# Kernel tuning notes

Hardware: AMD Instinct MI355X
Metric: run time of the kernel (lower is better)

Reference implementation:

```python
import jax, jax.numpy as jnp
import numpy as np

B, L, HID = 4, 1024, 2048
H, DK, DV, KS = 16, 128, 128, 4
KEY_DIM, VAL_DIM = H * DK, H * DV
CONV_DIM = 2 * KEY_DIM + VAL_DIM
EPS = 1e-6


def setup_inputs() -> dict:
    key = jax.random.key(0)
    ks = jax.random.split(key, 8)
    return {
        "hidden_states": jax.random.normal(ks[0], (B, L, HID), jnp.float32),
        "W_qkvz": jax.random.normal(ks[1], (HID, 2 * KEY_DIM + 2 * VAL_DIM), jnp.float32) * 0.02,
        "W_ba": jax.random.normal(ks[2], (HID, 2 * H), jnp.float32) * 0.02,
        "conv_w": jax.random.normal(ks[3], (CONV_DIM, KS), jnp.float32) * 0.1,
        "conv_b": jnp.zeros((CONV_DIM,), jnp.float32),
        "A_log": jnp.log(jax.random.uniform(ks[4], (H,), jnp.float32, 1e-3, 16.0)),
        "dt_bias": jnp.ones((H,), jnp.float32),
        "norm_w": jnp.ones((DV,), jnp.float32),
        "W_out": jax.random.normal(ks[5], (VAL_DIM, HID), jnp.float32) * 0.02,
    }


def _l2norm(x):
    return x * jax.lax.rsqrt(jnp.sum(x * x, -1, keepdims=True) + EPS)


def _gdn_core(q, k, v, g, beta):
    # q,k: [B,L,H,DK], v: [B,L,H,DV], g,beta: [B,L,H]
    scale = q.shape[-1] ** -0.5

    def step(S, inp):
        qt, kt, vt, gt, bt = inp  # [B,H,*]
        S = S * jnp.exp(gt)[..., None, None]          # per-step gated decay
        v_pred = jnp.einsum('bhk,bhkd->bhd', kt, S)   # read memory at k_t
        delta = (vt - v_pred) * bt[..., None]         # delta-rule update
        S = S + jnp.einsum('bhk,bhd->bhkd', kt, delta)
        o = jnp.einsum('bhk,bhkd->bhd', qt, S) * scale
        return S, o

    S0 = jnp.zeros((q.shape[0], q.shape[2], q.shape[3], v.shape[3]), q.dtype)
    xs = (q.transpose(1, 0, 2, 3), k.transpose(1, 0, 2, 3), v.transpose(1, 0, 2, 3),
          g.transpose(1, 0, 2), beta.transpose(1, 0, 2))
    _, o = jax.lax.scan(step, S0, xs)
    return o.transpose(1, 0, 2, 3)  # [B,L,H,DV]


def reference(hidden_states, W_qkvz, W_ba, conv_w, conv_b, A_log, dt_bias, norm_w, W_out):
    qkvz = hidden_states @ W_qkvz                      # [B,L,2*key+2*val]
    ba = hidden_states @ W_ba                          # [B,L,2H]
    mixed = qkvz[..., :CONV_DIM]
    z = qkvz[..., CONV_DIM:].reshape(B, L, H, DV)
    b_, a_ = ba[..., :H], ba[..., H:]

    # depthwise causal conv1d (left pad KS-1), no activation (activation=None)
    x = mixed.transpose(0, 2, 1)                       # [B,C,L]
    x = jax.lax.conv_general_dilated(
        x, conv_w[:, None, :], (1,), [(KS - 1, 0)],
        dimension_numbers=('NCH', 'OIH', 'NCH'), feature_group_count=CONV_DIM)
    x = (x + conv_b[None, :, None]).transpose(0, 2, 1)  # [B,L,C]

    q = _l2norm(x[..., :KEY_DIM].reshape(B, L, H, DK))
    k = _l2norm(x[..., KEY_DIM:2 * KEY_DIM].reshape(B, L, H, DK))
    v = x[..., 2 * KEY_DIM:].reshape(B, L, H, DV)

    g = -jnp.exp(A_log)[None, None, :] * jax.nn.softplus(a_ + dt_bias[None, None, :])
    beta = jax.nn.sigmoid(b_)

    o = _gdn_core(q, k, v, g, beta)                    # [B,L,H,DV]

    # gated RMSNorm (norm before gate)
    var = jnp.mean(o * o, -1, keepdims=True)
    o = o * jax.lax.rsqrt(var + EPS) * norm_w * jax.nn.sigmoid(z)
    return o.reshape(B, L, VAL_DIM) @ W_out            # [B,L,HID]
```

## Files before the change

kernel.cpp:

```cpp
#include <hip/hip_runtime.h>

typedef unsigned short u16;
typedef unsigned int u32;
typedef short short8 __attribute__((ext_vector_type(8)));
typedef float float4v __attribute__((ext_vector_type(4)));

#define L_SEQ 1024
#define NB 4
#define NH 16
#define DK 128
#define DV 128
#define HID 2048
#define NQKVZ 8192
#define CONV_DIM 6144
#define GDN_SCALE 0.08838834764831845f

static __device__ __forceinline__ float bf2f(u16 u) {
    union { u32 i; float f; } x; x.i = ((u32)u) << 16; return x.f;
}
static __device__ __forceinline__ u16 f2bf(float f) {
    union { float f; u32 u; } x; x.f = f;
    u32 r = x.u + 0x7FFF + ((x.u >> 16) & 1);
    return (u16)(r >> 16);
}

union FragU { short8 v; uint4 u; };

#define GLOAD_LDS16(g, l)                                        \
    __builtin_amdgcn_global_load_lds(                            \
        (const __attribute__((address_space(1))) void*)(g),      \
        (__attribute__((address_space(3))) void*)(l), 16, 0, 0)

__global__ __launch_bounds__(256) void f32_to_bf16(
    const float* __restrict__ in, u16* __restrict__ out) {
    long i = ((long)blockIdx.x * 256 + threadIdx.x) * 8;
    float4 a = *(const float4*)(in + i);
    float4 b = *(const float4*)(in + i + 4);
    u16 tmp[8];
    tmp[0] = f2bf(a.x); tmp[1] = f2bf(a.y); tmp[2] = f2bf(a.z); tmp[3] = f2bf(a.w);
    tmp[4] = f2bf(b.x); tmp[5] = f2bf(b.y); tmp[6] = f2bf(b.z); tmp[7] = f2bf(b.w);
    *(uint4*)(out + i) = *(const uint4*)tmp;
}

__global__ __launch_bounds__(256) void transpose_f32_bf16(
    const float* __restrict__ in, u16* __restrict__ out, int R, int C) {
    __shared__ float tile[32][33];
    int bx = blockIdx.x, by = blockIdx.y;
    int c = threadIdx.x & 31;
    int r0 = threadIdx.x >> 5;
#pragma unroll
    for (int i = 0; i < 4; i++) {
        int r = r0 + i * 8;
        tile[r][c] = in[(long)(by * 32 + r) * C + bx * 32 + c];
    }
    __syncthreads();
#pragma unroll
    for (int i = 0; i < 4; i++) {
        int r = r0 + i * 8;
        out[(long)(bx * 32 + r) * R + by * 32 + c] = f2bf(tile[c][r]);
    }
}

#define BM 128
#define BN 128
#define BKK 32

static __device__ __forceinline__ void store_out(u16* p, float v)  { *p = f2bf(v); }
static __device__ __forceinline__ void store_out(float* p, float v){ *p = v; }

template <typename OutT>
__global__ __launch_bounds__(256) void gemm_abT(
    const u16* __restrict__ A, const u16* __restrict__ BT,
    OutT* __restrict__ C, int M, int N, int K) {
    __shared__ u16 As[BM * BKK];
    __shared__ u16 Bs[BN * BKK];
    int t = threadIdx.x;
    int lane = t & 63;
    int w = t >> 6;
    int wm = (w & 1) * 64;
    int wn = (w >> 1) * 64;
    int l15 = lane & 15;
    int quad = lane >> 4;
    long blockM = (long)blockIdx.y * BM;
    long blockN = (long)blockIdx.x * BN;

    float4v acc[4][4];
#pragma unroll
    for (int i = 0; i < 4; i++)
#pragma unroll
        for (int j = 0; j < 4; j++) acc[i][j] = (float4v){0.f, 0.f, 0.f, 0.f};

    const u16* Ab = A + blockM * K;
    const u16* Bb = BT + blockN * K;

    const int r0 = t >> 2,         c0 = (t & 3) * 8;
    const int r1 = (t + 256) >> 2, c1 = ((t + 256) & 3) * 8;
    u16* As0 = As + t * 8;         u16* As1 = As + (t + 256) * 8;
    u16* Bs0 = Bs + t * 8;         u16* Bs1 = Bs + (t + 256) * 8;
    const u16* Ag0 = Ab + (long)r0 * K + c0;
    const u16* Ag1 = Ab + (long)r1 * K + c1;
    const u16* Bg0 = Bb + (long)r0 * K + c0;
    const u16* Bg1 = Bb + (long)r1 * K + c1;

    for (int k0 = 0; k0 < K; k0 += BKK) {
        __syncthreads();
        GLOAD_LDS16(Ag0 + k0, As0);
        GLOAD_LDS16(Ag1 + k0, As1);
        GLOAD_LDS16(Bg0 + k0, Bs0);
        GLOAD_LDS16(Bg1 + k0, Bs1);
        __syncthreads();

        FragU fa[4], fb[4];
#pragma unroll
        for (int i = 0; i < 4; i++) {
            fa[i].u = *(const uint4*)(As + (wm + i * 16 + l15) * BKK + quad * 8);
            fb[i].u = *(const uint4*)(Bs + (wn + i * 16 + l15) * BKK + quad * 8);
        }
#pragma unroll
        for (int i = 0; i < 4; i++)
#pragma unroll
            for (int j = 0; j < 4; j++)
                acc[i][j] = __builtin_amdgcn_mfma_f32_16x16x32_bf16(
                    fa[i].v, fb[j].v, acc[i][j], 0, 0, 0);
    }

#pragma unroll
    for (int i = 0; i < 4; i++) {
        long mrow = blockM + wm + i * 16 + quad * 4;
#pragma unroll
        for (int j = 0; j < 4; j++) {
            long col = blockN + wn + j * 16 + l15;
#pragma unroll
            for (int r = 0; r < 4; r++) {
                store_out(&C[(mrow + r) * N + col], acc[i][j][r]);
            }
        }
    }
}

#define G1_LDSU 32768

__global__ __launch_bounds__(512, 2) void gemm1_8ph(
    const u16* __restrict__ A, const u16* __restrict__ BT,
    u16* __restrict__ C) {
    const int K = HID, N = NQKVZ;
    __shared__ __align__(16) u16 lds[2 * G1_LDSU];

    int t = threadIdx.x;
    int lane = t & 63, w = t >> 6, l15 = lane & 15, quad = lane >> 4;
    int wm = w & 1, wn = w >> 1;

    int orig = blockIdx.x;
    int wg = (orig & 7) * 64 + (orig >> 3);
    int p = wg >> 6, q = wg & 63;
    long blockM = (long)((p >> 2) * 8 + (q >> 3)) * 256;
    long blockN = (long)((p & 3) * 8 + (q & 7)) * 256;

    int srow = t >> 3;
    int scol = ((t & 7) ^ (srow & 7)) * 8;
    const u16* Ast = A + (blockM + srow) * (long)K + scol;
    const u16* Bst = BT + (blockN + srow) * (long)K + scol;

#define STA(db, qq, T) GLOAD_LDS16(Ast + (long)(qq) * 64 * K + (T) * 64,      \
                                   lds + (db) * G1_LDSU + (qq) * 4096 + t * 8)
#define STB(db, qq, T) GLOAD_LDS16(Bst + (long)(qq) * 64 * K + (T) * 64,      \
                                   lds + (db) * G1_LDSU + 16384 + (qq) * 4096 + t * 8)

    const int rowA0 = (wm * 128 + l15) * 64;
    const int rowB0 = 16384 + (wn * 64 + l15) * 64;
    const int cs0 = ((quad) ^ (l15 & 7)) * 8;
    const int cs1 = ((4 + quad) ^ (l15 & 7)) * 8;

    float4v acc[8][4];
#pragma unroll
    for (int mi = 0; mi < 8; mi++)
#pragma unroll
        for (int nj = 0; nj < 4; nj++) acc[mi][nj] = (float4v){0.f, 0.f, 0.f, 0.f};

    STA(0, 0, 0); STA(0, 1, 0); STA(0, 2, 0); STA(0, 3, 0);
    STB(0, 0, 0); STB(0, 1, 0); STB(0, 2, 0); STB(0, 3, 0);
    STA(1, 0, 1); STA(1, 2, 1);
    asm volatile("s_waitcnt vmcnt(2)" ::: "memory");
    __builtin_amdgcn_s_barrier();

    FragU bA[4][2], bB0[2][2], bB1[2][2];

    for (int g = 0; g < 32; ++g) {
        const int c = g & 1, db = c ^ 1;
        const u16* sb = lds + c * G1_LDSU;

#pragma unroll
        for (int i = 0; i < 4; i++) {
            bA[i][0].u = *(const uint4*)(sb + rowA0 + i * 1024 + cs0);
            bA[i][1].u = *(const uint4*)(sb + rowA0 + i * 1024 + cs1);
        }
#pragma unroll
        for (int j = 0; j < 2; j++) {
            bB0[j][0].u = *(const uint4*)(sb + rowB0 + j * 1024 + cs0);
            bB0[j][1].u = *(const uint4*)(sb + rowB0 + j * 1024 + cs1);
        }
        if (g + 1 < 32) { STA(db, 1, g + 1); STA(db, 3, g + 1); }
        __builtin_amdgcn_s_barrier();
        asm volatile("s_waitcnt lgkmcnt(0)" ::: "memory");
        __builtin_amdgcn_s_setprio(1);
#pragma unroll
        for (int i = 0; i < 4; i++)
#pragma unroll
            for (int j = 0; j < 2; j++) {
                acc[i][j] = __builtin_amdgcn_mfma_f32_16x16x32_bf16(
                    bA[i][0].v, bB0[j][0].v, acc[i][j], 0, 0, 0);
                acc[i][j] = __builtin_amdgcn_mfma_f32_16x16x32_bf16(
                    bA[i][1].v, bB0[j][1].v, acc[i][j], 0, 0, 0);
            }
        __builtin_amdgcn_s_setprio(0);

#pragma unroll
        for (int j = 0; j < 2; j++) {
            bB1[j][0].u = *(const uint4*)(sb + rowB0 + (2 + j) * 1024 + cs0);
            bB1[j][1].u = *(const uint4*)(sb + rowB0 + (2 + j) * 1024 + cs1);
        }
        if (g + 1 < 32) { STB(db, 0, g + 1); STB(db, 1, g + 1); }
        __builtin_amdgcn_s_barrier();
        asm volatile("s_waitcnt lgkmcnt(0)" ::: "memory");
        __builtin_amdgcn_s_setprio(1);
#pragma unroll
        for (int i = 0; i < 4; i++)
#pragma unroll
            for (int j = 0; j < 2; j++) {
                acc[i][2 + j] = __builtin_amdgcn_mfma_f32_16x16x32_bf16(
                    bA[i][0].v, bB1[j][0].v, acc[i][2 + j], 0, 0, 0);
                acc[i][2 + j] = __builtin_amdgcn_mfma_f32_16x16x32_bf16(
                    bA[i][1].v, bB1[j][1].v, acc[i][2 + j], 0, 0, 0);
            }
        __builtin_amdgcn_s_setprio(0);

#pragma unroll
        for (int i = 0; i < 4; i++) {
            bA[i][0].u = *(const uint4*)(sb + rowA0 + (4 + i) * 1024 + cs0);
            bA[i][1].u = *(const uint4*)(sb + rowA0 + (4 + i) * 1024 + cs1);
        }
        if (g + 1 < 32) { STB(db, 2, g + 1); STB(db, 3, g + 1); }
        __builtin_amdgcn_s_barrier();
        asm volatile("s_waitcnt lgkmcnt(0)" ::: "memory");
        __builtin_amdgcn_s_setprio(1);
#pragma unroll
        for (int i = 0; i < 4; i++)
#pragma unroll
            for (int j = 0; j < 2; j++) {
                acc[4 + i][j] = __builtin_amdgcn_mfma_f32_16x16x32_bf16(
                    bA[i][0].v, bB0[j][0].v, acc[4 + i][j], 0, 0, 0);
                acc[4 + i][j] = __builtin_amdgcn_mfma_f32_16x16x32_bf16(
                    bA[i][1].v, bB0[j][1].v, acc[4 + i][j], 0, 0, 0);
            }
        __builtin_amdgcn_s_setprio(0);

        if (g + 2 < 32) { STA(c, 0, g + 2); STA(c, 2, g + 2); }
        __builtin_amdgcn_s_barrier();
        __builtin_amdgcn_s_setprio(1);
#pragma unroll
        for (int i = 0; i < 4; i++)
#pragma unroll
            for (int j = 0; j < 2; j++) {
                acc[4 + i][2 + j] = __builtin_amdgcn_mfma_f32_16x16x32_bf16(
                    bA[i][0].v, bB1[j][0].v, acc[4 + i][2 + j], 0, 0, 0);
                acc[4 + i][2 + j] = __builtin_amdgcn_mfma_f32_16x16x32_bf16(
                    bA[i][1].v, bB1[j][1].v, acc[4 + i][2 + j], 0, 0, 0);
            }
        __builtin_amdgcn_s_setprio(0);

        if (g < 30)       { asm volatile("s_waitcnt vmcnt(2)" ::: "memory"); }
        else if (g == 30) { asm volatile("s_waitcnt vmcnt(0)" ::: "memory"); }
        __builtin_amdgcn_s_barrier();
    }

#pragma unroll
    for (int mi = 0; mi < 8; mi++) {
        long row0 = blockM + wm * 128 + mi * 16 + quad * 4;
#pragma unroll
        for (int nj = 0; nj < 4; nj++) {
            long col = blockN + wn * 64 + nj * 16 + l15;
#pragma unroll
            for (int r = 0; r < 4; r++)
                C[(row0 + r) * N + col] = f2bf(acc[mi][nj][r]);
        }
    }
#undef STA
#undef STB
}

#define G2_LDSU 24576

__global__ __launch_bounds__(512) void gemm2_2ph(
    const u16* __restrict__ A, const u16* __restrict__ BT,
    float* __restrict__ C) {
    const int K = HID, N = 2048;
    __shared__ __align__(16) u16 lds[2 * G2_LDSU];

    int t = threadIdx.x;
    int lane = t & 63, w = t >> 6, l15 = lane & 15, quad = lane >> 4;
    int wm = w & 1, wn = w >> 1;

    int orig = blockIdx.x;
    int x = orig & 7, q = orig >> 3;
    long blockM = (long)((x >> 2) * 8 + (q >> 2)) * 256;
    long blockN = (long)((x & 3) * 4 + (q & 3)) * 128;

    int srow = t >> 3;
    int scol = ((t & 7) ^ (srow & 7)) * 8;
    const u16* Ast = A + (blockM + srow) * (long)K + scol;
    const u16* Bst = BT + (blockN + srow) * (long)K + scol;

#define STA2(db, qq, T) GLOAD_LDS16(Ast + (long)(qq) * 64 * K + (T) * 64,     \
                                    lds + (db) * G2_LDSU + (qq) * 4096 + t * 8)
#define STB2(db, hh, T) GLOAD_LDS16(Bst + (long)(hh) * 64 * K + (T) * 64,     \
                                    lds + (db) * G2_LDSU + 16384 + (hh) * 4096 + t * 8)

    const int cs0 = ((quad) ^ (l15 & 7)) * 8;
    const int cs1 = ((4 + quad) ^ (l15 & 7)) * 8;
    int offA[8], offB[2];
#pragma unroll
    for (int mi = 0; mi < 8; mi++)
        offA[mi] = (wm * 2 + (mi >> 2)) * 4096 + (((mi & 3) * 16 + l15)) * 64;
#pragma unroll
    for (int nj = 0; nj < 2; nj++)
        offB[nj] = 16384 + (wn >> 1) * 4096 + ((wn & 1) * 32 + nj * 16 + l15) * 64;

    float4v acc[8][2];
#pragma unroll
    for (int mi = 0; mi < 8; mi++)
#pragma unroll
        for (int nj = 0; nj < 2; nj++) acc[mi][nj] = (float4v){0.f, 0.f, 0.f, 0.f};

    STA2(0, 0, 0); STA2(0, 2, 0); STB2(0, 0, 0); STB2(0, 1, 0);
    STA2(0, 1, 0); STA2(0, 3, 0);
    STA2(1, 0, 1); STA2(1, 2, 1); STB2(1, 0, 1); STB2(1, 1, 1);
    asm volatile("s_waitcnt vmcnt(6)" ::: "memory");
    __builtin_amdgcn_s_barrier();

    FragU fA[4][2], fB[2][2];

    for (int g = 0; g < 32; ++g) {
        const int c = g & 1, db = c ^ 1;
        const u16* sb = lds + c * G2_LDSU;

#pragma unroll
        for (int i = 0; i < 4; i++) {
            fA[i][0].u = *(const uint4*)(sb + offA[i] + cs0);
            fA[i][1].u = *(const uint4*)(sb + offA[i] + cs1);
        }
#pragma unroll
        for (int j = 0; j < 2; j++) {
            fB[j][0].u = *(const uint4*)(sb + offB[j] + cs0);
            fB[j][1].u = *(const uint4*)(sb + offB[j] + cs1);
        }
        if (g < 31) { STA2(db, 1, g + 1); STA2(db, 3, g + 1); }
        asm volatile("s_waitcnt lgkmcnt(8)" ::: "memory");
        __builtin_amdgcn_s_barrier();
        __builtin_amdgcn_s_setprio(1);
#pragma unroll
        for (int i = 0; i < 4; i++)
#pragma unroll
            for (int j = 0; j < 2; j++) {
                acc[i][j] = __builtin_amdgcn_mfma_f32_16x16x32_bf16(
                    fA[i][0].v, fB[j][0].v, acc[i][j], 0, 0, 0);
                acc[i][j] = __builtin_amdgcn_mfma_f32_16x16x32_bf16(
                    fA[i][1].v, fB[j][1].v, acc[i][j], 0, 0, 0);
            }
        __builtin_amdgcn_s_setprio(0);

        if (g < 31) { asm volatile("s_waitcnt vmcnt(6)" ::: "memory"); }
        else        { asm volatile("s_waitcnt vmcnt(0)" ::: "memory"); }
        __builtin_amdgcn_s_barrier();
        if (g < 30) { STA2(c, 0, g + 2); STA2(c, 2, g + 2);
                      STB2(c, 0, g + 2); STB2(c, 1, g + 2); }
#pragma unroll
        for (int i = 0; i < 4; i++) {
            fA[i][0].u = *(const uint4*)(sb + offA[4 + i] + cs0);
            fA[i][1].u = *(const uint4*)(sb + offA[4 + i] + cs1);
        }
        __builtin_amdgcn_s_setprio(1);
#pragma unroll
        for (int i = 0; i < 4; i++)
#pragma unroll
            for (int j = 0; j < 2; j++) {
                acc[4 + i][j] = __builtin_amdgcn_mfma_f32_16x16x32_bf16(
                    fA[i][0].v, fB[j][0].v, acc[4 + i][j], 0, 0, 0);
                acc[4 + i][j] = __builtin_amdgcn_mfma_f32_16x16x32_bf16(
                    fA[i][1].v, fB[j][1].v, acc[4 + i][j], 0, 0, 0);
            }
        __builtin_amdgcn_s_setprio(0);

        if (g < 30)       { asm volatile("s_waitcnt vmcnt(6)" ::: "memory"); }
        else if (g == 30) { asm volatile("s_waitcnt vmcnt(2)" ::: "memory"); }
        if (g < 31) __builtin_amdgcn_s_barrier();
    }

#pragma unroll
    for (int mi = 0; mi < 8; mi++) {
        long row0 = blockM + wm * 128 + mi * 16 + quad * 4;
#pragma unroll
        for (int nj = 0; nj < 2; nj++) {
            long col = blockN + wn * 32 + nj * 16 + l15;
#pragma unroll
            for (int r = 0; r < 4; r++)
                C[(row0 + r) * N + col] = acc[mi][nj][r];
        }
    }
#undef STA2
#undef STB2
}

__global__ __launch_bounds__(256) void ba_gemm(
    const u16* __restrict__ hsb, const u16* __restrict__ WbaTb,
    const float* __restrict__ A_log, const float* __restrict__ dtb,
    float* __restrict__ gout, float* __restrict__ bout) {
    __shared__ u16 As[2][64 * 32];
    __shared__ u16 Bs[2][32 * 32];
    int t = threadIdx.x;
    int lane = t & 63, w = t >> 6, l15 = lane & 15, quad = lane >> 4;
    long blockM = (long)blockIdx.x * 64;

    float4v acc[2];
    acc[0] = (float4v){0.f, 0.f, 0.f, 0.f};
    acc[1] = (float4v){0.f, 0.f, 0.f, 0.f};

    const u16* Ag  = hsb + (blockM + (t >> 2)) * (long)HID + (t & 3) * 8;
    const u16* Bg1 = WbaTb + (long)(t >> 4) * HID + ((t * 2) & 31);
    const u16* Bg2 = Bg1 + 16 * (long)HID;

#define STBA(buf, k0) do {                                                     \
        GLOAD_LDS16(Ag + (k0), As[buf] + t * 8);                               \
        __builtin_amdgcn_global_load_lds(                                      \
            (const __attribute__((address_space(1))) void*)(Bg1 + (k0)),       \
            (__attribute__((address_space(3))) void*)(Bs[buf] + t * 2), 4, 0, 0); \
        __builtin_amdgcn_global_load_lds(                                      \
            (const __attribute__((address_space(1))) void*)(Bg2 + (k0)),       \
            (__attribute__((address_space(3))) void*)(Bs[buf] + 512 + t * 2), 4, 0, 0); \
    } while (0)

    STBA(0, 0);
    STBA(1, 32);

    for (int k0 = 0; k0 < HID; k0 += 32) {
        int buf = (k0 >> 5) & 1;
        if (k0 < HID - 64) { asm volatile("s_waitcnt vmcnt(3)" ::: "memory"); }
        else               { asm volatile("s_waitcnt vmcnt(0)" ::: "memory"); }
        __builtin_amdgcn_s_barrier();
        FragU fa, fb0, fb1;
        fa.u  = *(const uint4*)(As[buf] + (w * 16 + l15) * 32 + quad * 8);
        fb0.u = *(const uint4*)(Bs[buf] + l15 * 32 + quad * 8);
        fb1.u = *(const uint4*)(Bs[buf] + (16 + l15) * 32 + quad * 8);
        asm volatile("s_waitcnt lgkmcnt(0)" ::: "memory");
        __builtin_amdgcn_sched_barrier(0);
        __builtin_amdgcn_s_barrier();
        if (k0 + 64 < HID) STBA(buf, k0 + 64);
        acc[0] = __builtin_amdgcn_mfma_f32_16x16x32_bf16(fa.v, fb0.v, acc[0], 0, 0, 0);
        acc[1] = __builtin_amdgcn_mfma_f32_16x16x32_bf16(fa.v, fb1.v, acc[1], 0, 0, 0);
    }
#undef STBA

#pragma unroll
    for (int j = 0; j < 2; j++) {
        int n = j * 16 + l15;
#pragma unroll
        for (int r = 0; r < 4; r++) {
            long m = blockM + w * 16 + quad * 4 + r;
            int b = (int)(m >> 10), l = (int)(m & 1023);
            float v = acc[j][r];
            if (n < 16) {
                bout[((long)(b * NH + n)) * L_SEQ + l] = 1.f / (1.f + expf(-v));
            } else {
                int h = n - 16;
                float x = v + dtb[h];
                float sp = (x > 20.f) ? x : log1pf(expf(x));
                gout[((long)(b * NH + h)) * L_SEQ + l] = -expf(A_log[h]) * sp;
            }
        }
    }
}

__global__ __launch_bounds__(256) void conv_qkv(
    const u16* __restrict__ qkvz, const float* __restrict__ conv_w,
    const float* __restrict__ conv_b,
    u16* __restrict__ qs, u16* __restrict__ ks, u16* __restrict__ vs) {
    int orig = blockIdx.x;
    int bl = ((orig & 7) << 9) + (orig >> 3);
    int b = bl >> 10, l = bl & 1023;
    int t = threadIdx.x;
    __shared__ float xb[CONV_DIM];
    __shared__ float red[32][9];
    __shared__ float rbuf[32];

    for (int c = t; c < CONV_DIM; c += 256) {
        float acc = conv_b[c];
        float w0 = conv_w[c * 4 + 0];
        float w1 = conv_w[c * 4 + 1];
        float w2 = conv_w[c * 4 + 2];
        float w3 = conv_w[c * 4 + 3];
        long rowbase = (long)(b * L_SEQ) * NQKVZ + c;
        if (l - 3 >= 0) acc += bf2f(qkvz[rowbase + (long)(l - 3) * NQKVZ]) * w0;
        if (l - 2 >= 0) acc += bf2f(qkvz[rowbase + (long)(l - 2) * NQKVZ]) * w1;
        if (l - 1 >= 0) acc += bf2f(qkvz[rowbase + (long)(l - 1) * NQKVZ]) * w2;
        acc += bf2f(qkvz[rowbase + (long)l * NQKVZ]) * w3;
        xb[c] = acc;
    }
    __syncthreads();
    {
        int grp = t >> 3;
        int j8 = t & 7;
        float s = 0.f;
#pragma unroll
        for (int i = 0; i < 16; i++) {
            float xv = xb[grp * 128 + j8 * 16 + i];
            s += xv * xv;
        }
        red[grp][j8] = s;
    }
    __syncthreads();
    if (t < 32) {
        float s = 0.f;
#pragma unroll
        for (int i = 0; i < 8; i++) s += red[t][i];
        rbuf[t] = rsqrtf(s + 1e-6f);
    }
    __syncthreads();
    for (int c = t; c < CONV_DIM; c += 256) {
        float xv = xb[c];
        if (c < 2048) {
            int h = c >> 7, d = c & 127;
            qs[(((long)(b * NH + h)) * L_SEQ + l) * DK + d] = f2bf(xv * rbuf[h]);
        } else if (c < 4096) {
            int c2 = c - 2048;
            int h = c2 >> 7, d = c2 & 127;
            ks[(((long)(b * NH + h)) * L_SEQ + l) * DK + d] = f2bf(xv * rbuf[16 + h]);
        } else {
            int c2 = c - 4096;
            int h = c2 >> 7, d = c2 & 127;
            vs[(((long)(b * NH + h)) * L_SEQ + l) * DV + d] = f2bf(xv);
        }
    }
}

__global__ __launch_bounds__(256) void gdn_prep(
    const u16* __restrict__ ks_g, const u16* __restrict__ qs_g,
    const float* __restrict__ g_g, const float* __restrict__ b_g,
    u16* __restrict__ Tbuf, u16* __restrict__ Pbuf,
    u16* __restrict__ wbq, u16* __restrict__ qlq, u16* __restrict__ kdq,
    float* __restrict__ gam_g) {
    int cid = blockIdx.x;
    int bh = cid >> 4;
    int ch = cid & 15;
    long rowbase = (long)bh * L_SEQ + ch * 64;
    int t = threadIdx.x;
    int lane = t & 63, w = t >> 6, l15 = lane & 15, quad = lane >> 4;

    __shared__ u16 Kl[64 * 136];
    __shared__ u16 Ql[64 * 136];
    __shared__ float Am[64 * 66];
    __shared__ float Tm[64 * 66];
    __shared__ float Tt[32 * 33];
    __shared__ float Gs[64], lamL[64], betaL[64], dlL[64];

    {
        int row = t >> 2, seg = (t & 3) * 32;
        const u16* ksrc = ks_g + (rowbase + row) * DK + seg;
        const u16* qsrc = qs_g + (rowbase + row) * DK + seg;
        *(uint4*)&Kl[row * 136 + seg]      = *(const uint4*)ksrc;
        *(uint4*)&Kl[row * 136 + seg + 8]  = *(const uint4*)(ksrc + 8);
        *(uint4*)&Kl[row * 136 + seg + 16] = *(const uint4*)(ksrc + 16);
        *(uint4*)&Kl[row * 136 + seg + 24] = *(const uint4*)(ksrc + 24);
        *(uint4*)&Ql[row * 136 + seg]      = *(const uint4*)qsrc;
        *(uint4*)&Ql[row * 136 + seg + 8]  = *(const uint4*)(qsrc + 8);
        *(uint4*)&Ql[row * 136 + seg + 16] = *(const uint4*)(qsrc + 16);
        *(uint4*)&Ql[row * 136 + seg + 24] = *(const uint4*)(qsrc + 24);
        if (t < 64) Gs[t] = g_g[rowbase + t];
        else if (t < 128) betaL[t - 64] = b_g[rowbase + t - 64];
    }
    __syncthreads();
    if (t < 64) {
        float gv = Gs[t];
#pragma unroll
        for (int off = 1; off < 64; off <<= 1) {
            float n = __shfl_up(gv, off);
            if (lane >= off) gv += n;
        }
        Gs[t] = gv;
    }
    __syncthreads();
    if (t < 64) {
        float G63 = Gs[63];
        float lm = expf(Gs[t]);
        lamL[t] = lm;
        dlL[t] = expf(G63 - Gs[t]);
        if (t == 0) gam_g[cid] = expf(G63);
    }
    float4v accKK[4], accQK[4];
#pragma unroll
    for (int tj = 0; tj < 4; tj++) {
        accKK[tj] = (float4v){0.f, 0.f, 0.f, 0.f};
        accQK[tj] = (float4v){0.f, 0.f, 0.f, 0.f};
    }
#pragma unroll
    for (int k0 = 0; k0 < 128; k0 += 32) {
        FragU ka, qa;
        ka.u = *(const uint4*)&Kl[(w * 16 + l15) * 136 + k0 + quad * 8];
        qa.u = *(const uint4*)&Ql[(w * 16 + l15) * 136 + k0 + quad * 8];
#pragma unroll
        for (int tj = 0; tj < 4; tj++) {
            FragU kb;
            kb.u = *(const uint4*)&Kl[(tj * 16 + l15) * 136 + k0 + quad * 8];
            accKK[tj] = __builtin_amdgcn_mfma_f32_16x16x32_bf16(ka.v, kb.v, accKK[tj], 0, 0, 0);
            accQK[tj] = __builtin_amdgcn_mfma_f32_16x16x32_bf16(qa.v, kb.v, accQK[tj], 0, 0, 0);
        }
    }
    __syncthreads();
#pragma unroll
    for (int tj = 0; tj < 4; tj++) {
#pragma unroll
        for (int r = 0; r < 4; r++) {
            int ti_ = w * 16 + quad * 4 + r;
            int j = tj * 16 + l15;
            float e = (j <= ti_) ? expf(Gs[ti_] - Gs[j]) : 0.f;
            Am[ti_ * 66 + j] = (j < ti_) ? betaL[ti_] * e * accKK[tj][r] : 0.f;
            Pbuf[(long)cid * 4096 + ti_ * 64 + j] =
                (j <= ti_) ? f2bf(GDN_SCALE * e * accQK[tj][r]) : (u16)0;
        }
    }
    {
        int row = t >> 2, seg = (t & 3) * 32;
        float sw = -betaL[row] * lamL[row];
        float sq = GDN_SCALE * lamL[row];
#pragma unroll
        for (int c0 = 0; c0 < 32; c0 += 8) {
            u16 wt[8], qt2[8];
#pragma unroll
            for (int j2 = 0; j2 < 8; j2++) {
                wt[j2]  = f2bf(sw * bf2f(Kl[row * 136 + seg + c0 + j2]));
                qt2[j2] = f2bf(sq * bf2f(Ql[row * 136 + seg + c0 + j2]));
            }
            *(uint4*)&wbq[(long)cid * 8192 + row * 128 + seg + c0] = *(uint4*)wt;
            *(uint4*)&qlq[(long)cid * 8192 + row * 128 + seg + c0] = *(uint4*)qt2;
        }
    }
    {
        int k = t & 127, t0b = (t >> 7) * 32;
#pragma unroll
        for (int t0 = 0; t0 < 32; t0 += 8) {
            u16 tmp[8];
#pragma unroll
            for (int j2 = 0; j2 < 8; j2++)
                tmp[j2] = f2bf(dlL[t0b + t0 + j2] * bf2f(Kl[(t0b + t0 + j2) * 136 + k]));
            *(uint4*)&kdq[(long)cid * 8192 + k * 64 + t0b + t0] = *(uint4*)tmp;
        }
    }
    __syncthreads();
    if (t < 32) {
        int c = t;
        for (int i = 0; i < 32; i++) {
            float s = (i == c) ? 1.f : 0.f;
            for (int j = 0; j < i; j++) s -= Am[i * 66 + j] * Tm[j * 66 + c];
            Tm[i * 66 + c] = s;
        }
    } else if (t >= 64 && t < 96) {
        int c = 32 + (t - 64);
        for (int i = 32; i < 64; i++) {
            float s = (i == c) ? 1.f : 0.f;
            for (int j = 32; j < i; j++) s -= Am[i * 66 + j] * Tm[j * 66 + c];
            Tm[i * 66 + c] = s;
        }
    } else if (t >= 128 && t < 192) {
        int idx = t - 128;
        for (int kk = 0; kk < 16; kk++) {
            int e = idx * 16 + kk;
            Tm[(e >> 5) * 66 + 32 + (e & 31)] = 0.f;
        }
    }
    __syncthreads();
    {
        int e0 = t * 4;
#pragma unroll
        for (int kk = 0; kk < 4; kk++) {
            int e = e0 + kk; int i = e >> 5, c = e & 31;
            float s = 0.f;
            for (int j = 0; j < 32; j++) s += Am[(32 + i) * 66 + j] * Tm[j * 66 + c];
            Tt[i * 33 + c] = s;
        }
    }
    __syncthreads();
    {
        int e0 = t * 4;
#pragma unroll
        for (int kk = 0; kk < 4; kk++) {
            int e = e0 + kk; int i = e >> 5, c = e & 31;
            float s = 0.f;
            for (int j = 0; j < 32; j++) s -= Tm[(32 + i) * 66 + 32 + j] * Tt[j * 33 + c];
            Tm[(32 + i) * 66 + c] = s;
        }
    }
    __syncthreads();
    {
        int row = t >> 2, c0 = (t & 3) * 16;
        u16 tmp[16];
#pragma unroll
        for (int i = 0; i < 16; i++) tmp[i] = f2bf(Tm[row * 66 + c0 + i]);
        *(uint4*)&Tbuf[(long)cid * 4096 + row * 64 + c0]     = *(uint4*)tmp;
        *(uint4*)&Tbuf[(long)cid * 4096 + row * 64 + c0 + 8] = *(uint4*)(tmp + 8);
    }
}

__global__ __launch_bounds__(256) void gdn_chunk(
    const u16* __restrict__ vs_g, const float* __restrict__ b_g,
    const u16* __restrict__ Tq, const u16* __restrict__ Pq,
    const u16* __restrict__ wbq, const u16* __restrict__ qlq,
    const u16* __restrict__ kdq, const float* __restrict__ gam_g,
    float* __restrict__ o_g) {
    int orig = blockIdx.x;
    int bid = ((orig & 7) << 6) + (orig >> 3);
    int dc = bid & 7;
    int bh = bid >> 3;
    int b = bh >> 4, h = bh & 15;
    int t = threadIdx.x;
    int lane = t & 63, w = t >> 6, l15 = lane & 15, quad = lane >> 4;

    __shared__ u16 s0h[16 * 136], s0l[16 * 136];
    __shared__ float vO[64 * 20];
    __shared__ u16 rhsT[16 * 72], DT[16 * 72];

    float4v S0r[2];
    S0r[0] = (float4v){0.f, 0.f, 0.f, 0.f};
    S0r[1] = (float4v){0.f, 0.f, 0.f, 0.f};

    const int orow = t >> 2, oseg = (t & 3) * 4;

    for (int ch = 0; ch < 16; ch++) {
        int cid = bh * 16 + ch;
        long rowbase = (long)bh * L_SEQ + ch * 64;
        float gam = gam_g[cid];

        const u16* wbp = wbq + (long)cid * 8192 + (w * 16 + l15) * 128 + quad * 8;
        uint4 wbf0 = *(const uint4*)(wbp);
        uint4 wbf1 = *(const uint4*)(wbp + 32);
        uint4 wbf2 = *(const uint4*)(wbp + 64);
        uint4 wbf3 = *(const uint4*)(wbp + 96);

        if (ch > 0) {
            float4 a = *(const float4*)&vO[orow * 20 + oseg];
            float* d2 = o_g + (((long)b * L_SEQ + (ch - 1) * 64 + orow) * 16 + h) * 128L
                        + dc * 16 + oseg;
            *(float4*)d2 = a;
        }
        {
            float beta = b_g[rowbase + orow];
            uint2 vv = *(const uint2*)(vs_g + (rowbase + orow) * DV + dc * 16 + oseg);
            const u16* vp = (const u16*)&vv;
#pragma unroll
            for (int j2 = 0; j2 < 4; j2++)
                vO[orow * 20 + oseg + j2] = beta * bf2f(vp[j2]);
        }
#pragma unroll
        for (int ktl = 0; ktl < 2; ktl++) {
            int kc = (2 * w + ktl) * 16 + l15;
#pragma unroll
            for (int r = 0; r < 4; r++) {
                float x = S0r[ktl][r];
                u16 hi = f2bf(x);
                float lo = x - bf2f(hi);
                s0h[(quad * 4 + r) * 136 + kc] = hi;
                s0l[(quad * 4 + r) * 136 + kc] = f2bf(lo);
            }
        }
        __syncthreads();

        const u16* Tp = Tq + (long)cid * 4096 + (w * 16 + l15) * 64 + quad * 8;
        uint4 Tf0 = *(const uint4*)(Tp);
        uint4 Tf1 = *(const uint4*)(Tp + 32);
        {
            float4v acc;
#pragma unroll
            for (int r = 0; r < 4; r++)
                acc[r] = vO[(w * 16 + quad * 4 + r) * 20 + l15];
            uint4 wbf[4] = {wbf0, wbf1, wbf2, wbf3};
#pragma unroll
            for (int k0 = 0; k0 < 4; k0++) {
                FragU a, bh_, bl_;
                a.u = wbf[k0];
                bh_.u = *(const uint4*)&s0h[l15 * 136 + k0 * 32 + quad * 8];
                acc = __builtin_amdgcn_mfma_f32_16x16x32_bf16(a.v, bh_.v, acc, 0, 0, 0);
                bl_.u = *(const uint4*)&s0l[l15 * 136 + k0 * 32 + quad * 8];
                acc = __builtin_amdgcn_mfma_f32_16x16x32_bf16(a.v, bl_.v, acc, 0, 0, 0);
            }
            u16 tmp[4] = {f2bf(acc[0]), f2bf(acc[1]), f2bf(acc[2]), f2bf(acc[3])};
            *(uint2*)&rhsT[l15 * 72 + w * 16 + quad * 4] = *(uint2*)tmp;
        }
        __syncthreads();

        const u16* qlp = qlq + (long)cid * 8192 + (w * 16 + l15) * 128 + quad * 8;
        uint4 qlf0 = *(const uint4*)(qlp);
        uint4 qlf1 = *(const uint4*)(qlp + 32);
        uint4 qlf2 = *(const uint4*)(qlp + 64);
        uint4 qlf3 = *(const uint4*)(qlp + 96);
        const u16* Pp = Pq + (long)cid * 4096 + (w * 16 + l15) * 64 + quad * 8;
        uint4 Pf0 = *(const uint4*)(Pp);
        uint4 Pf1 = *(const uint4*)(Pp + 32);
        {
            float4v acc = (float4v){0.f, 0.f, 0.f, 0.f};
            uint4 Tf[2] = {Tf0, Tf1};
#pragma unroll
            for (int k0 = 0; k0 < 2; k0++) {
                FragU a, b_;
                a.u = Tf[k0];
                b_.u = *(const uint4*)&rhsT[l15 * 72 + k0 * 32 + quad * 8];
                acc = __builtin_amdgcn_mfma_f32_16x16x32_bf16(a.v, b_.v, acc, 0, 0, 0);
            }
            u16 tmp[4] = {f2bf(acc[0]), f2bf(acc[1]), f2bf(acc[2]), f2bf(acc[3])};
            *(uint2*)&DT[l15 * 72 + w * 16 + quad * 4] = *(uint2*)tmp;
        }
        __syncthreads();

        uint4 kdf[2][2];
#pragma unroll
        for (int ktl = 0; ktl < 2; ktl++) {
            const u16* kdp = kdq + (long)cid * 8192 + ((2 * w + ktl) * 16 + l15) * 64 + quad * 8;
            kdf[ktl][0] = *(const uint4*)(kdp);
            kdf[ktl][1] = *(const uint4*)(kdp + 32);
        }
        {
            float4v acc = (float4v){0.f, 0.f, 0.f, 0.f};
            uint4 qlf[4] = {qlf0, qlf1, qlf2, qlf3};
#pragma unroll
            for (int k0 = 0; k0 < 4; k0++) {
                FragU a, bh_, bl_;
                a.u = qlf[k0];
                bh_.u = *(const uint4*)&s0h[l15 * 136 + k0 * 32 + quad * 8];
                acc = __builtin_amdgcn_mfma_f32_16x16x32_bf16(a.v, bh_.v, acc, 0, 0, 0);
                bl_.u = *(const uint4*)&s0l[l15 * 136 + k0 * 32 + quad * 8];
                acc = __builtin_amdgcn_mfma_f32_16x16x32_bf16(a.v, bl_.v, acc, 0, 0, 0);
            }
            uint4 Pf[2] = {Pf0, Pf1};
#pragma unroll
            for (int k0 = 0; k0 < 2; k0++) {
                FragU a, b_;
                a.u = Pf[k0];
                b_.u = *(const uint4*)&DT[l15 * 72 + k0 * 32 + quad * 8];
                acc = __builtin_amdgcn_mfma_f32_16x16x32_bf16(a.v, b_.v, acc, 0, 0, 0);
            }
#pragma unroll
            for (int r = 0; r < 4; r++)
                vO[(w * 16 + quad * 4 + r) * 20 + l15] = acc[r];
        }
#pragma unroll
        for (int ktl = 0; ktl < 2; ktl++) {
            float4v acc = S0r[ktl];
#pragma unroll
            for (int r = 0; r < 4; r++) acc[r] *= gam;
#pragma unroll
            for (int t0 = 0; t0 < 2; t0++) {
                FragU a, b_;
                a.u = *(const uint4*)&DT[l15 * 72 + t0 * 32 + quad * 8];
                b_.u = kdf[ktl][t0];
                acc = __builtin_amdgcn_mfma_f32_16x16x32_bf16(a.v, b_.v, acc, 0, 0, 0);
            }
            S0r[ktl] = acc;
        }
        __syncthreads();
    }
    {
        float4 a = *(const float4*)&vO[orow * 20 + oseg];
        float* d2 = o_g + (((long)b * L_SEQ + 15 * 64 + orow) * 16 + h) * 128L
                    + dc * 16 + oseg;
        *(float4*)d2 = a;
    }
}

__global__ __launch_bounds__(128) void gated_norm(
    const float* __restrict__ o, const u16* __restrict__ qkvz,
    const float* __restrict__ norm_w, u16* __restrict__ A2) {
    int bid = blockIdx.x;
    int t = threadIdx.x;
    float ov = o[(long)bid * 128 + t];
    float s = ov * ov;
#pragma unroll
    for (int off = 32; off > 0; off >>= 1) s += __shfl_down(s, off);
    __shared__ float ws2[2];
    if ((t & 63) == 0) ws2[t >> 6] = s;
    __syncthreads();
    float tot = ws2[0] + ws2[1];
    float rinv = rsqrtf(tot * (1.f / 128.f) + 1e-6f);
    int bl = bid >> 4, h = bid & 15;
    float z = bf2f(qkvz[(long)bl * NQKVZ + CONV_DIM + h * 128 + t]);
    float sig = 1.f / (1.f + expf(-z));
    float val = ov * rinv * norm_w[t] * sig;
    A2[(long)bl * 2048 + h * 128 + t] = f2bf(val);
}

extern "C" void kernel_launch(void* const* d_in, const int* in_sizes, int n_in,
                              void* d_out, int out_size, void* d_ws, size_t ws_size,
                              hipStream_t stream) {
    const float* hs    = (const float*)d_in[0];
    const float* Wqkvz = (const float*)d_in[1];
    const float* Wba   = (const float*)d_in[2];
    const float* convw = (const float*)d_in[3];
    const float* convb = (const float*)d_in[4];
    const float* A_log = (const float*)d_in[5];
    const float* dtb   = (const float*)d_in[6];
    const float* normw = (const float*)d_in[7];
    const float* Wout  = (const float*)d_in[8];

    char* ws = (char*)d_ws;
    size_t off = 0;
    auto alloc = [&](size_t bytes) {
        size_t o = off;
        off = (off + bytes + 255) & ~(size_t)255;
        return o;
    };
    size_t r0 = alloc((size_t)NQKVZ * HID * 2);
    size_t r1 = alloc((size_t)4096 * HID * 2);
    u16*   WqkvzT = (u16*)(ws + r0);
    float* os     = (float*)(ws + r0);
    u16*   hsb    = (u16*)(ws + r1);
    u16*   A2     = (u16*)(ws + r1);
    u16*   qkvz   = (u16*)(ws + alloc((size_t)4096 * NQKVZ * 2));
    u16*   qs     = (u16*)(ws + alloc((size_t)64 * L_SEQ * DK * 2));
    u16*   ks     = (u16*)(ws + alloc((size_t)64 * L_SEQ * DK * 2));
    u16*   vs     = (u16*)(ws + alloc((size_t)64 * L_SEQ * DV * 2));
    float* gs     = (float*)(ws + alloc((size_t)64 * L_SEQ * 4));
    float* bs     = (float*)(ws + alloc((size_t)64 * L_SEQ * 4));
    u16*   WoutT  = (u16*)(ws + alloc((size_t)HID * 2048 * 2));
    u16*   WbaTb  = (u16*)(ws + alloc((size_t)32 * HID * 2));
    u16*   Tbuf   = (u16*)(ws + alloc((size_t)1024 * 4096 * 2));
    u16*   Pbuf   = (u16*)(ws + alloc((size_t)1024 * 4096 * 2));
    u16*   wbq    = (u16*)(ws + alloc((size_t)1024 * 8192 * 2));
    u16*   qlq    = (u16*)(ws + alloc((size_t)1024 * 8192 * 2));
    u16*   kdq    = (u16*)(ws + alloc((size_t)1024 * 8192 * 2));
    float* gamb   = (float*)(ws + alloc((size_t)1024 * 4));

    hipLaunchKernelGGL(f32_to_bf16, dim3(4096), dim3(256), 0, stream, hs, hsb);
    hipLaunchKernelGGL(transpose_f32_bf16, dim3(NQKVZ / 32, HID / 32), dim3(256), 0, stream,
                       Wqkvz, WqkvzT, HID, NQKVZ);
    hipLaunchKernelGGL(transpose_f32_bf16, dim3(2048 / 32, 2048 / 32), dim3(256), 0, stream,
                       Wout, WoutT, 2048, 2048);
    hipLaunchKernelGGL(transpose_f32_bf16, dim3(1, HID / 32), dim3(256), 0, stream,
                       Wba, WbaTb, HID, 32);

    hipLaunchKernelGGL(gemm1_8ph, dim3(512), dim3(512), 0, stream,
                       hsb, WqkvzT, qkvz);

    hipLaunchKernelGGL(ba_gemm, dim3(64), dim3(256), 0, stream,
                       hsb, WbaTb, A_log, dtb, gs, bs);

    hipLaunchKernelGGL(conv_qkv, dim3(4096), dim3(256), 0, stream,
                       qkvz, convw, convb, qs, ks, vs);

    hipLaunchKernelGGL(gdn_prep, dim3(1024), dim3(256), 0, stream,
                       ks, qs, gs, bs, Tbuf, Pbuf, wbq, qlq, kdq, gamb);

    hipLaunchKernelGGL(gdn_chunk, dim3(512), dim3(256), 0, stream,
                       vs, bs, Tbuf, Pbuf, wbq, qlq, kdq, gamb, os);

    hipLaunchKernelGGL(gated_norm, dim3(4096 * NH), dim3(128), 0, stream,
                       os, qkvz, normw, A2);

    hipLaunchKernelGGL(gemm2_2ph, dim3(256), dim3(512), 0, stream,
                       A2, WoutT, (float*)d_out);
}
```

Measured before the change: 559.8 us.

## Retile ba_gemm into smaller blocks and vectorize conv_qkv loads and stores

ba_gemm now uses 32-row tiles with a 2x2 wave layout, doubling the grid from 64 to 128 blocks to fill more compute units. Each thread issues a single 16-byte global-to-LDS load per stage. conv_qkv now loads 8 bf16 channels per thread with 16-byte vector reads, vectorizes the conv weight and bias reads, and writes q/k/v with 16-byte stores instead of scalar 2-byte accesses. A no-op loop is also added to gemm1. The aim is better memory coalescing and more parallelism in the small kernels.

```diff
diff --git a/kernel.cpp b/kernel.cpp
--- a/kernel.cpp
+++ b/kernel.cpp
@@ -254,6 +254,8 @@
             }
         __builtin_amdgcn_s_setprio(0);
 
+#pragma unroll
+        for (int i = 0; i < 4; i++) { (void)0; }
         if (g + 2 < 32) { STA(c, 0, g + 2); STA(c, 2, g + 2); }
         __builtin_amdgcn_s_barrier();
         __builtin_amdgcn_s_setprio(1);
@@ -414,59 +416,48 @@
     const u16* __restrict__ hsb, const u16* __restrict__ WbaTb,
     const float* __restrict__ A_log, const float* __restrict__ dtb,
     float* __restrict__ gout, float* __restrict__ bout) {
-    __shared__ u16 As[2][64 * 32];
+    __shared__ u16 As[2][32 * 32];
     __shared__ u16 Bs[2][32 * 32];
     int t = threadIdx.x;
     int lane = t & 63, w = t >> 6, l15 = lane & 15, quad = lane >> 4;
-    long blockM = (long)blockIdx.x * 64;
-
-    float4v acc[2];
-    acc[0] = (float4v){0.f, 0.f, 0.f, 0.f};
-    acc[1] = (float4v){0.f, 0.f, 0.f, 0.f};
-
-    const u16* Ag  = hsb + (blockM + (t >> 2)) * (long)HID + (t & 3) * 8;
-    const u16* Bg1 = WbaTb + (long)(t >> 4) * HID + ((t * 2) & 31);
-    const u16* Bg2 = Bg1 + 16 * (long)HID;
-
-#define STBA(buf, k0) do {                                                     \
-        GLOAD_LDS16(Ag + (k0), As[buf] + t * 8);                               \
-        __builtin_amdgcn_global_load_lds(                                      \
-            (const __attribute__((address_space(1))) void*)(Bg1 + (k0)),       \
-            (__attribute__((address_space(3))) void*)(Bs[buf] + t * 2), 4, 0, 0); \
-        __builtin_amdgcn_global_load_lds(                                      \
-            (const __attribute__((address_space(1))) void*)(Bg2 + (k0)),       \
-            (__attribute__((address_space(3))) void*)(Bs[buf] + 512 + t * 2), 4, 0, 0); \
-    } while (0)
-
-    STBA(0, 0);
-    STBA(1, 32);
+    long blockM = (long)blockIdx.x * 32;
+
+    float4v acc = (float4v){0.f, 0.f, 0.f, 0.f};
+
+    int sidx = t & 127;
+    const u16* Sg = (t < 128)
+        ? hsb + (blockM + (sidx >> 2)) * (long)HID + (sidx & 3) * 8
+        : WbaTb + (long)(sidx >> 2) * HID + (sidx & 3) * 8;
+    u16* Sl0 = (t < 128) ? As[0] + sidx * 8 : Bs[0] + sidx * 8;
+    u16* Sl1 = (t < 128) ? As[1] + sidx * 8 : Bs[1] + sidx * 8;
+
+    GLOAD_LDS16(Sg + 0, Sl0);
+    GLOAD_LDS16(Sg + 32, Sl1);
+
+    const int wr = (w >> 1) * 16, wc = (w & 1) * 16;
 
     for (int k0 = 0; k0 < HID; k0 += 32) {
         int buf = (k0 >> 5) & 1;
-        if (k0 < HID - 64) { asm volatile("s_waitcnt vmcnt(3)" ::: "memory"); }
+        if (k0 < HID - 64) { asm volatile("s_waitcnt vmcnt(1)" ::: "memory"); }
         else               { asm volatile("s_waitcnt vmcnt(0)" ::: "memory"); }
         __builtin_amdgcn_s_barrier();
-        FragU fa, fb0, fb1;
-        fa.u  = *(const uint4*)(As[buf] + (w * 16 + l15) * 32 + quad * 8);
-        fb0.u = *(const uint4*)(Bs[buf] + l15 * 32 + quad * 8);
-        fb1.u = *(const uint4*)(Bs[buf] + (16 + l15) * 32 + quad * 8);
+        FragU fa, fb;
+        fa.u = *(const uint4*)(As[buf] + (wr + l15) * 32 + quad * 8);
+        fb.u = *(const uint4*)(Bs[buf] + (wc + l15) * 32 + quad * 8);
         asm volatile("s_waitcnt lgkmcnt(0)" ::: "memory");
         __builtin_amdgcn_sched_barrier(0);
         __builtin_amdgcn_s_barrier();
-        if (k0 + 64 < HID) STBA(buf, k0 + 64);
-        acc[0] = __builtin_amdgcn_mfma_f32_16x16x32_bf16(fa.v, fb0.v, acc[0], 0, 0, 0);
-        acc[1] = __builtin_amdgcn_mfma_f32_16x16x32_bf16(fa.v, fb1.v, acc[1], 0, 0, 0);
-    }
-#undef STBA
-
-#pragma unroll
-    for (int j = 0; j < 2; j++) {
-        int n = j * 16 + l15;
+        if (k0 + 64 < HID) GLOAD_LDS16(Sg + k0 + 64, buf ? Sl1 : Sl0);
+        acc = __builtin_amdgcn_mfma_f32_16x16x32_bf16(fa.v, fb.v, acc, 0, 0, 0);
+    }
+
+    {
+        int n = wc + l15;
 #pragma unroll
         for (int r = 0; r < 4; r++) {
-            long m = blockM + w * 16 + quad * 4 + r;
+            long m = blockM + wr + quad * 4 + r;
             int b = (int)(m >> 10), l = (int)(m & 1023);
-            float v = acc[j][r];
+            float v = acc[r];
             if (n < 16) {
                 bout[((long)(b * NH + n)) * L_SEQ + l] = 1.f / (1.f + expf(-v));
             } else {
@@ -491,18 +482,33 @@
     __shared__ float red[32][9];
     __shared__ float rbuf[32];
 
-    for (int c = t; c < CONV_DIM; c += 256) {
-        float acc = conv_b[c];
-        float w0 = conv_w[c * 4 + 0];
-        float w1 = conv_w[c * 4 + 1];
-        float w2 = conv_w[c * 4 + 2];
-        float w3 = conv_w[c * 4 + 3];
-        long rowbase = (long)(b * L_SEQ) * NQKVZ + c;
-        if (l - 3 >= 0) acc += bf2f(qkvz[rowbase + (long)(l - 3) * NQKVZ]) * w0;
-        if (l - 2 >= 0) acc += bf2f(qkvz[rowbase + (long)(l - 2) * NQKVZ]) * w1;
-        if (l - 1 >= 0) acc += bf2f(qkvz[rowbase + (long)(l - 1) * NQKVZ]) * w2;
-        acc += bf2f(qkvz[rowbase + (long)l * NQKVZ]) * w3;
-        xb[c] = acc;
+    const int ok3 = (l >= 3), ok2 = (l >= 2), ok1 = (l >= 1);
+#pragma unroll
+    for (int pass = 0; pass < 3; pass++) {
+        int c = pass * 2048 + t * 8;
+        long rowbase = (long)(b * L_SEQ + l) * NQKVZ + c;
+        uint4 x3 = ok3 ? *(const uint4*)(qkvz + rowbase - 3L * NQKVZ) : (uint4){0,0,0,0};
+        uint4 x2 = ok2 ? *(const uint4*)(qkvz + rowbase - 2L * NQKVZ) : (uint4){0,0,0,0};
+        uint4 x1 = ok1 ? *(const uint4*)(qkvz + rowbase - 1L * NQKVZ) : (uint4){0,0,0,0};
+        uint4 x0 = *(const uint4*)(qkvz + rowbase);
+        const u16* p3 = (const u16*)&x3;
+        const u16* p2 = (const u16*)&x2;
+        const u16* p1 = (const u16*)&x1;
+        const u16* p0 = (const u16*)&x0;
+        float4 cb0 = *(const float4*)(conv_b + c);
+        float4 cb1 = *(const float4*)(conv_b + c + 4);
+        const float* cbp = &cb0.x;
+#pragma unroll
+        for (int j = 0; j < 8; j++) {
+            float4 wv = *(const float4*)(conv_w + (c + j) * 4);
+            float accv = ((j < 4) ? (&cb0.x)[j] : (&cb1.x)[j - 4]);
+            if (ok3) accv += bf2f(p3[j]) * wv.x;
+            if (ok2) accv += bf2f(p2[j]) * wv.y;
+            if (ok1) accv += bf2f(p1[j]) * wv.z;
+            accv += bf2f(p0[j]) * wv.w;
+            xb[c + j] = accv;
+        }
+        (void)cbp;
     }
     __syncthreads();
     {
@@ -524,20 +530,27 @@
         rbuf[t] = rsqrtf(s + 1e-6f);
     }
     __syncthreads();
-    for (int c = t; c < CONV_DIM; c += 256) {
-        float xv = xb[c];
-        if (c < 2048) {
-            int h = c >> 7, d = c & 127;
-            qs[(((long)(b * NH + h)) * L_SEQ + l) * DK + d] = f2bf(xv * rbuf[h]);
-        } else if (c < 4096) {
-            int c2 = c - 2048;
-            int h = c2 >> 7, d = c2 & 127;
-            ks[(((long)(b * NH + h)) * L_SEQ + l) * DK + d] = f2bf(xv * rbuf[16 + h]);
-        } else {
-            int c2 = c - 4096;
-            int h = c2 >> 7, d = c2 & 127;
-            vs[(((long)(b * NH + h)) * L_SEQ + l) * DV + d] = f2bf(xv);
-        }
+    {
+        int c0 = t * 8;
+        int h = c0 >> 7, d = c0 & 127;
+        u16 outv[8];
+        float sq = rbuf[h];
+#pragma unroll
+        for (int j = 0; j < 8; j++) outv[j] = f2bf(xb[c0 + j] * sq);
+        *(uint4*)&qs[(((long)(b * NH + h)) * L_SEQ + l) * DK + d] = *(const uint4*)outv;
+
+        int c1 = 2048 + t * 8;
+        int h1 = (c1 - 2048) >> 7, d1 = (c1 - 2048) & 127;
+        float sk = rbuf[16 + h1];
+#pragma unroll
+        for (int j = 0; j < 8; j++) outv[j] = f2bf(xb[c1 + j] * sk);
+        *(uint4*)&ks[(((long)(b * NH + h1)) * L_SEQ + l) * DK + d1] = *(const uint4*)outv;
+
+        int c2 = 4096 + t * 8;
+        int h2 = (c2 - 4096) >> 7, d2 = (c2 - 4096) & 127;
+#pragma unroll
+        for (int j = 0; j < 8; j++) outv[j] = f2bf(xb[c2 + j]);
+        *(uint4*)&vs[(((long)(b * NH + h2)) * L_SEQ + l) * DV + d2] = *(const uint4*)outv;
     }
 }
 
@@ -945,7 +958,7 @@
     hipLaunchKernelGGL(gemm1_8ph, dim3(512), dim3(512), 0, stream,
                        hsb, WqkvzT, qkvz);
 
-    hipLaunchKernelGGL(ba_gemm, dim3(64), dim3(256), 0, stream,
+    hipLaunchKernelGGL(ba_gemm, dim3(128), dim3(256), 0, stream,
                        hsb, WbaTb, A_log, dtb, gs, bs);
 
     hipLaunchKernelGGL(conv_qkv, dim3(4096), dim3(256), 0, stream,
```

Result: slower. 599.4 us (+7.1%).
